# Kernel optimization log

Hardware: AMD Instinct MI355X
Metric: run time of the kernel (lower is better)

## Reference

```python
import jax, jax.numpy as jnp
import numpy as np

N = 4096
DEG = 16.0
KC = 64  # max closed-neighborhood size supported (deg~16 graph => safe)


def setup_inputs() -> dict:
    key = jax.random.key(0)
    ks = jax.random.split(key, 6)
    u = jax.random.uniform(ks[0], (N, N))
    upper = jnp.triu((u < (DEG / N)).astype(jnp.float32), k=1)
    adj = upper + upper.T  # symmetric 0/1, zero diagonal
    d = 64
    return {
        'adj': adj,
        'e_w': jax.random.normal(ks[1], (15, d), dtype=jnp.float32) * 0.25,
        'e_b': jnp.zeros((d,), jnp.float32),
        'w1': jax.random.normal(ks[2], (3, d, d), dtype=jnp.float32) * 0.125,
        'b1': jnp.zeros((3, d), jnp.float32),
        'w2': jax.random.normal(ks[3], (3, d, d), dtype=jnp.float32) * 0.125,
        'b2': jnp.zeros((3, d), jnp.float32),
        'eps': jnp.zeros((3,), jnp.float32),
    }


def cr_feat(adj):
    n = adj.shape[0]
    m = adj + jnp.eye(n, dtype=adj.dtype)  # closed-neighborhood indicator rows [N,N]
    k = m.sum(1)                            # |S_v|
    D = m @ adj                             # D[v,u] = degree of u inside S_v (A symmetric)
    E = 0.5 * jnp.sum(m * D, axis=1)        # edges inside S_v
    W = jnp.sum(m * D * (D - 1.0) * 0.5, axis=1)  # wedges inside S_v
    vals, idx = jax.lax.top_k(m, KC)        # members of S_v (padded)
    valid = (vals > 0.5).astype(adj.dtype)
    sub = adj[idx[:, :, None], idx[:, None, :]]        # [N,KC,KC] induced subgraph
    sub = sub * valid[:, :, None] * valid[:, None, :]
    T = jnp.einsum('vij,vjk,vki->v', sub, sub, sub) / 6.0  # triangles inside S_v
    f3 = T
    f2 = W - 3.0 * T
    f1 = E * (k - 2.0) - 2.0 * f2 - 3.0 * f3
    tot = k * (k - 1.0) * (k - 2.0) / 6.0   # C(k,3) = total triples
    f0 = tot - f1 - f2 - f3
    f = jnp.stack([f0, f1, f2, f3], axis=1)
    f = jnp.where((k >= 3.0)[:, None], f, 0.0)  # original skips |nb|<3
    return f / (jnp.sum(f, axis=1, keepdims=True) + 1e-10)


def ww_feat(adj):
    a2 = adj @ adj
    a4 = a2 @ a2                             # matrix_power(adj, 4)
    vals, _ = jax.lax.top_k(a4, 8)           # per-row sort desc, top 8
    return vals


def degree_feat(adj):
    d = adj.sum(1)
    diag_a2 = jnp.einsum('vu,uv->v', adj, adj)  # diag(A@A)
    return jnp.stack([d, d ** 2, diag_a2], axis=1)


def _forward(adj, e_w, e_b, w1, b1, w2, b2, eps):
    feats = jnp.concatenate([cr_feat(adj), ww_feat(adj), degree_feat(adj)], axis=1)  # [N,15]
    x = feats @ e_w + e_b
    for i in range(3):
        h = (1.0 + eps[i]) * x + adj @ x
        x = jax.nn.relu(h @ w1[i] + b1[i]) @ w2[i] + b2[i]
    return x.sum(0)


def reference(adj, e_w, e_b, w1, b1, w2, b2, eps):
    return _forward(adj, e_w, e_b, w1, b1, w2, b2, eps)
```

## Files before the change

### kernel.cpp

```cpp
#include <hip/hip_runtime.h>
#include <hip/hip_bf16.h>
#include <stdint.h>

#define NN 4096
#define MAXNZ 1536


__global__ __launch_bounds__(256) void scan_k(const float* __restrict__ adj,
                                              int* __restrict__ nbr,
                                              int* __restrict__ deg,
                                              unsigned long long* __restrict__ abits,
                                              float* __restrict__ feats) {
    __shared__ int nlist[4][64];
    int tid = threadIdx.x;
    int wv = tid >> 6, ln = tid & 63;
    int v = blockIdx.x * 4 + wv;
    size_t rb = (size_t)v * NN;
    int total = 0;
    unsigned long long w0 = 0;
    const float4* row4 = (const float4*)(adj + rb);
    for (int base = 0; base < NN; base += 256) {
        float4 f = row4[(base >> 2) + ln];
        int q4 = (base >> 8) << 2;
        #pragma unroll
        for (int j = 0; j < 4; j++) {
            float vj = (j == 0) ? f.x : (j == 1) ? f.y : (j == 2) ? f.z : f.w;
            unsigned long long m = __ballot(vj > 0.5f);
            if (vj > 0.5f) {
                int pos = total + __popcll(m & ((1ull << ln) - 1ull));
                if (pos < 64) nlist[wv][pos] = base + 4 * ln + j;
            }
            if (ln == q4 + j) w0 = m;
            total += __popcll(m);
        }
    }
    abits[(size_t)v * 64 + ln] = w0;
    int degL = min(total, 64);
    if (ln < degL) nbr[v * 64 + ln] = nlist[wv][ln];
    if (ln == 0) {
        deg[v] = total;
        float degf = (float)total;
        feats[v * 16 + 12] = degf;
        feats[v * 16 + 13] = degf * degf;
        feats[v * 16 + 14] = degf;
    }
}

__global__ __launch_bounds__(256) void cra2_k(const unsigned long long* __restrict__ abits,
                                              const int* __restrict__ nbr,
                                              const int* __restrict__ deg,
                                              unsigned int* __restrict__ csr,
                                              int* __restrict__ cnt,
                                              unsigned char* __restrict__ ncb,
                                              float* __restrict__ feats) {
    __shared__ __align__(16) unsigned int smem[NN + 264];
    int tid = threadIdx.x;
    int bid = blockIdx.x;
    int wv = tid >> 6, ln = tid & 63;

    if (bid < NN) {
        unsigned int* acc   = smem;
        int* us             = (int*)(smem + NN);
        int* dus            = (int*)(smem + NN + 64);
        unsigned int* cntS  = smem + NN;
        unsigned int* wsumS = smem + NN + 256;
        int v = bid;
        {
            uint4 z = {0u, 0u, 0u, 0u};
            #pragma unroll
            for (int i = 0; i < 4; i++) ((uint4*)acc)[tid + 256 * i] = z;
        }
        int dv = min(deg[v], 64);
        if (tid < dv) {
            int u = nbr[v * 64 + tid];
            us[tid] = u;
            dus[tid] = min(deg[u], 64);
        }
        __syncthreads();
        for (int p = tid; p < dv * 64; p += 256) {
            int i = p >> 6, wi = p & 63;
            int u = us[i];
            if (wi < dus[i]) atomicAdd(&acc[nbr[u * 64 + wi]], 1u);
        }
        __syncthreads();
        unsigned int local = 0;
        #pragma unroll
        for (int m = 0; m < 16; m++) {
            unsigned int a = acc[tid + 256 * m];
            local += (a + 14u) / 15u;
        }
        int rank = (tid & 31) * 8 + (tid >> 5);
        cntS[rank] = local;
        __syncthreads();
        unsigned int vmy = cntS[tid];
        unsigned int incl = vmy;
        #pragma unroll
        for (int off = 1; off < 64; off <<= 1) {
            unsigned int n = (unsigned int)__shfl_up((int)incl, off, 64);
            if (ln >= off) incl += n;
        }
        if (ln == 63) wsumS[wv] = incl;
        __syncthreads();
        unsigned int wprefix = 0, tot = 0;
        #pragma unroll
        for (int q = 0; q < 4; q++) {
            unsigned int s = wsumS[q];
            if (q < wv) wprefix += s;
            tot += s;
        }
        cntS[tid] = wprefix + (incl - vmy);
        __syncthreads();
        unsigned int pos = cntS[rank];
        unsigned short* dst = (unsigned short*)((char*)csr + (size_t)v * 3072);
        #pragma unroll
        for (int m = 0; m < 16; m++) {
            unsigned int a = acc[tid + 256 * m];
            unsigned int col = (unsigned int)(tid + 256 * m);
            while (a) {
                unsigned int w = a > 15u ? 15u : a;
                if (pos < 1520u) dst[pos] = (unsigned short)((w << 12) | col);
                pos++;
                a -= w;
            }
        }
        unsigned int bs = min(tot, 1520u);
        unsigned int padto = (bs + 7u) & ~7u;
        if (tid < padto - bs) dst[bs + tid] = (unsigned short)(bs + tid);
        if (tid == 0) {
            cnt[v] = (int)bs;
            ncb[v] = (unsigned char)(padto >> 3);
        }
    } else {
        unsigned long long* rows = (unsigned long long*)smem;
        int* mems = (int*)(smem + 1024);
        int v = (bid - NN) * 4 + wv;

        int dv = deg[v];
        int degL = min(dv, 64);
        int c = min(dv + 1, 64);

        int nl = (ln < degL) ? nbr[v * 64 + ln] : 0;
        int isless = (ln < degL && nl < v) ? 1 : 0;
        int pos = isless;
        #pragma unroll
        for (int off = 32; off; off >>= 1) pos += __shfl_xor(pos, off, 64);

        int mem = 0;
        if (ln < c) {
            if (ln < pos)       mem = nl;
            else if (ln == pos) mem = v;
            else                mem = nbr[v * 64 + ln - 1];
        }
        mems[wv * 64 + ln] = mem;
        __syncthreads();

        unsigned long long mask = 0ull;
        {
            const unsigned long long* rowb = abits + (size_t)mem * 64;
            for (int j = 0; j < c; j++) {
                int mj = mems[wv * 64 + j];
                unsigned long long w = rowb[((mj >> 8) << 2) | (mj & 3)];
                mask |= ((w >> ((mj >> 2) & 63)) & 1ull) << j;
            }
        }
        if (ln >= c) mask = 0ull;
        rows[wv * 64 + ln] = mask;
        __syncthreads();

        int tpart = 0;
        float epart = 0.f, wpart = 0.f;
        if (ln < c) {
            unsigned long long mm = mask;
            while (mm) {
                int j = __ffsll(mm) - 1;
                mm &= mm - 1;
                tpart += __popcll(mask & rows[wv * 64 + j]);
            }
            if (ln != pos) {
                int cn = __popcll(rows[wv * 64 + pos] & mask);
                float D2 = (float)cn + 1.0f;
                epart = D2;
                wpart = D2 * (D2 - 1.0f) * 0.5f;
            }
        }
        float es = epart, wsum2 = wpart;
        int ts = tpart;
        #pragma unroll
        for (int off = 32; off; off >>= 1) {
            es += __shfl_xor(es, off, 64);
            wsum2 += __shfl_xor(wsum2, off, 64);
            ts += __shfl_xor(ts, off, 64);
        }

        if (ln == 0) {
            float degf = (float)dv;
            float k = degf + 1.0f;
            float E = 0.5f * (es + degf);
            float W = wsum2 + degf * (degf - 1.0f) * 0.5f;
            float T = (float)ts / 6.0f;
            float f3 = T;
            float f2 = W - 3.0f * T;
            float f1 = E * (k - 2.0f) - 2.0f * f2 - 3.0f * f3;
            float tot2 = k * (k - 1.0f) * (k - 2.0f) / 6.0f;
            float f0 = tot2 - f1 - f2 - f3;
            if (k < 3.0f) { f0 = f1 = f2 = f3 = 0.f; }
            float s = f0 + f1 + f2 + f3 + 1e-10f;
            feats[v * 16 + 0] = f0 / s;
            feats[v * 16 + 1] = f1 / s;
            feats[v * 16 + 2] = f2 / s;
            feats[v * 16 + 3] = f3 / s;
        }
    }
}

__global__ __launch_bounds__(1024) void order_k(const unsigned char* __restrict__ ncb,
                                                int* __restrict__ ord) {
    __shared__ unsigned int bcnt[192];
    __shared__ unsigned int bbase[192];
    int tid = threadIdx.x;
    if (tid < 192) bcnt[tid] = 0u;
    __syncthreads();
    unsigned char myk[4];
    #pragma unroll
    for (int j = 0; j < 4; j++) {
        int v = tid * 4 + j;
        myk[j] = ncb[v];
        atomicAdd(&bcnt[myk[j]], 1u);
    }
    __syncthreads();
    if (tid == 0) {
        unsigned int run = 0;
        for (int b = 191; b >= 0; b--) { bbase[b] = run; run += bcnt[b]; }
    }
    __syncthreads();
    #pragma unroll
    for (int j = 0; j < 4; j++) {
        int v = tid * 4 + j;
        unsigned int p = atomicAdd(&bbase[myk[j]], 1u);
        ord[p] = v;
    }
}

__device__ __forceinline__ void do8(unsigned int* acc, uint4 E, unsigned int W) {
    atomicAdd(&acc[E.x & 0xFFFu],         W * ((E.x >> 12) & 0xFu));
    atomicAdd(&acc[(E.x >> 16) & 0xFFFu], W * (E.x >> 28));
    atomicAdd(&acc[E.y & 0xFFFu],         W * ((E.y >> 12) & 0xFu));
    atomicAdd(&acc[(E.y >> 16) & 0xFFFu], W * (E.y >> 28));
    atomicAdd(&acc[E.z & 0xFFFu],         W * ((E.z >> 12) & 0xFu));
    atomicAdd(&acc[(E.z >> 16) & 0xFFFu], W * (E.z >> 28));
    atomicAdd(&acc[E.w & 0xFFFu],         W * ((E.w >> 12) & 0xFu));
    atomicAdd(&acc[(E.w >> 16) & 0xFFFu], W * (E.w >> 28));
}

__device__ __forceinline__ void do8_1(unsigned int* acc, uint4 E) {
    atomicAdd(&acc[E.x & 0xFFFu],         (E.x >> 12) & 0xFu);
    atomicAdd(&acc[(E.x >> 16) & 0xFFFu], E.x >> 28);
    atomicAdd(&acc[E.y & 0xFFFu],         (E.y >> 12) & 0xFu);
    atomicAdd(&acc[(E.y >> 16) & 0xFFFu], E.y >> 28);
    atomicAdd(&acc[E.z & 0xFFFu],         (E.z >> 12) & 0xFu);
    atomicAdd(&acc[(E.z >> 16) & 0xFFFu], E.z >> 28);
    atomicAdd(&acc[E.w & 0xFFFu],         (E.w >> 12) & 0xFu);
    atomicAdd(&acc[(E.w >> 16) & 0xFFFu], E.w >> 28);
}

__global__ __launch_bounds__(512) void a4row_k(const unsigned int* __restrict__ csr,
                                               const int* __restrict__ cnt,
                                               const unsigned char* __restrict__ ncb,
                                               const int* __restrict__ ord,
                                               const float* __restrict__ feats,
                                               const float* __restrict__ e_w,
                                               const float* __restrict__ e_b,
                                               float* __restrict__ x0) {
    __shared__ unsigned int acc[NN];
    __shared__ __align__(16) unsigned int rowe[MAXNZ];
    __shared__ unsigned int wtops[64];
    int tid = threadIdx.x;
    int wv = tid >> 6, ln = tid & 63;
    int v = ord[blockIdx.x];

    {
        uint4 z = {0u, 0u, 0u, 0u};
        #pragma unroll
        for (int i = 0; i < 2; i++) ((uint4*)acc)[tid + 512 * i] = z;
    }

    int nv = cnt[v];
    int nvp = (nv + 7) & ~7;
    const unsigned short* rowv = (const unsigned short*)((const char*)csr + (size_t)v * 3072);
    for (int i = tid; i < nvp; i += 512) {
        unsigned int e = rowv[i];
        unsigned int u = e & 0xFFFu;
        unsigned int w = e >> 12;
        unsigned int nc = w ? (unsigned int)ncb[u] : 0u;
        rowe[i] = u | (w << 12) | (nc << 16);
    }
    __syncthreads();

    const uint4* csr4 = (const uint4*)csr;
    for (int i0 = wv * 4; i0 < nvp; i0 += 32) {
        uint4 q = *(const uint4*)&rowe[i0];
        int c1 = (int)(q.x >> 16);
        int c2 = c1 + (int)(q.y >> 16);
        int c3 = c2 + (int)(q.z >> 16);
        int tot = c3 + (int)(q.w >> 16);
        unsigned int s0 = ((q.x & 0xFFFu) * 192u)                                 | (((q.x >> 12) & 0xFu) << 21);
        unsigned int s1 = (((q.y & 0xFFFu) * 192u - (unsigned int)c1) & 0x1FFFFFu) | (((q.y >> 12) & 0xFu) << 21);
        unsigned int s2 = (((q.z & 0xFFFu) * 192u - (unsigned int)c2) & 0x1FFFFFu) | (((q.z >> 12) & 0xFu) << 21);
        unsigned int s3 = (((q.w & 0xFFFu) * 192u - (unsigned int)c3) & 0x1FFFFFu) | (((q.w >> 12) & 0xFu) << 21);
        if (((q.x | q.y | q.z | q.w) & 0xF000u) == 0x1000u) {
            for (int g = ln; g < tot; g += 64) {
                unsigned int sel = (g < c1) ? s0 : ((g < c2) ? s1 : ((g < c3) ? s2 : s3));
                unsigned int idx = (sel + (unsigned int)g) & 0x1FFFFFu;
                uint4 E = csr4[idx];
                do8_1(acc, E);
            }
        } else {
            for (int g = ln; g < tot; g += 64) {
                unsigned int sel = (g < c1) ? s0 : ((g < c2) ? s1 : ((g < c3) ? s2 : s3));
                unsigned int idx = (sel + (unsigned int)g) & 0x1FFFFFu;
                uint4 E = csr4[idx];
                do8(acc, E, sel >> 21);
            }
        }
    }
    __syncthreads();

    unsigned int best[8];
    #pragma unroll
    for (int q = 0; q < 8; q++) best[q] = 0u;
    #pragma unroll
    for (int m = 0; m < 8; m++) {
        unsigned int val = acc[tid + 512 * m];
        if (val > best[7]) {
            best[7] = val;
            #pragma unroll
            for (int s = 7; s > 0; s--) {
                if (best[s] > best[s - 1]) {
                    unsigned int t2 = best[s - 1]; best[s - 1] = best[s]; best[s] = t2;
                } else break;
            }
        }
    }

    unsigned int wave_val = 0u;
    #pragma unroll
    for (int r = 0; r < 8; r++) {
        unsigned int m = best[0];
        #pragma unroll
        for (int off = 32; off; off >>= 1)
            m = max(m, (unsigned int)__shfl_xor((int)m, off, 64));
        unsigned long long bb = __ballot(best[0] == m);
        int src = __ffsll(bb) - 1;
        if (ln == src) {
            #pragma unroll
            for (int s = 0; s < 7; s++) best[s] = best[s + 1];
            best[7] = 0u;
        }
        if (ln == r) wave_val = m;
    }
    if (ln < 8) wtops[wv * 8 + ln] = wave_val;
    __syncthreads();

    if (wv == 0) {
        unsigned int cand = wtops[ln];
        unsigned int myv = 0u;
        #pragma unroll
        for (int r = 0; r < 8; r++) {
            unsigned int m = cand;
            #pragma unroll
            for (int off = 32; off; off >>= 1)
                m = max(m, (unsigned int)__shfl_xor((int)m, off, 64));
            unsigned long long bb = __ballot(cand == m);
            int src = __ffsll(bb) - 1;
            if (ln == src) cand = 0u;
            if (ln == r) myv = m;
        }
        int d = ln;
        float s = e_b[d];
        s += feats[v * 16 + 0]  * e_w[0 * 64 + d];
        s += feats[v * 16 + 1]  * e_w[1 * 64 + d];
        s += feats[v * 16 + 2]  * e_w[2 * 64 + d];
        s += feats[v * 16 + 3]  * e_w[3 * 64 + d];
        #pragma unroll
        for (int j = 0; j < 8; j++) {
            float mj = (float)(unsigned int)__shfl((int)myv, j, 64);
            s += mj * e_w[(4 + j) * 64 + d];
        }
        s += feats[v * 16 + 12] * e_w[12 * 64 + d];
        s += feats[v * 16 + 13] * e_w[13 * 64 + d];
        s += feats[v * 16 + 14] * e_w[14 * 64 + d];
        x0[(size_t)v * 64 + d] = s;
    }
}

__global__ __launch_bounds__(256) void layer_k(const float* __restrict__ xin,
                                               float* __restrict__ xout,
                                               const float* __restrict__ w1,
                                               const float* __restrict__ b1,
                                               const float* __restrict__ w2,
                                               const float* __restrict__ b2,
                                               const float* __restrict__ eps,
                                               const int* __restrict__ nbr,
                                               const int* __restrict__ deg,
                                               float* __restrict__ out,
                                               int li) {
    __shared__ float wL[4096];
    __shared__ float h[4][64], t[4][64];
    int tid = threadIdx.x;
    int wv = tid >> 6, d = tid & 63;
    int v = blockIdx.x * 4 + wv;

    {
        const float4* src = (const float4*)(w1 + li * 4096);
        #pragma unroll
        for (int i = 0; i < 4; i++) ((float4*)wL)[tid + 256 * i] = src[tid + 256 * i];
    }

    float xv = xin[(size_t)v * 64 + d];
    int dv = min(deg[v], 64);
    const int* nl = nbr + v * 64;
    float agg = 0.f;
    int j = 0;
    for (; j + 4 <= dv; j += 4) {
        int n0 = nl[j], n1 = nl[j + 1], n2 = nl[j + 2], n3 = nl[j + 3];
        float a0 = xin[(size_t)n0 * 64 + d];
        float a1 = xin[(size_t)n1 * 64 + d];
        float a2v = xin[(size_t)n2 * 64 + d];
        float a3 = xin[(size_t)n3 * 64 + d];
        agg += (a0 + a1) + (a2v + a3);
    }
    for (; j < dv; j++) agg += xin[(size_t)nl[j] * 64 + d];
    float hv = (1.0f + eps[li]) * xv + agg;
    h[wv][d] = hv;
    __syncthreads();

    float s = b1[li * 64 + d];
    #pragma unroll 8
    for (int k = 0; k < 64; k++) s += h[wv][k] * wL[k * 64 + d];
    s = fmaxf(s, 0.f);
    t[wv][d] = s;
    __syncthreads();

    {
        const float4* src = (const float4*)(w2 + li * 4096);
        #pragma unroll
        for (int i = 0; i < 4; i++) ((float4*)wL)[tid + 256 * i] = src[tid + 256 * i];
    }
    __syncthreads();

    float o = b2[li * 64 + d];
    #pragma unroll 8
    for (int k = 0; k < 64; k++) o += t[wv][k] * wL[k * 64 + d];
    if (li == 2) {
        h[wv][d] = o;
        __syncthreads();
        if (wv == 0)
            atomicAdd(&out[d], (h[0][d] + h[1][d]) + (h[2][d] + h[3][d]));
    } else {
        xout[(size_t)v * 64 + d] = o;
    }
}

extern "C" void kernel_launch(void* const* d_in, const int* in_sizes, int n_in,
                              void* d_out, int out_size, void* d_ws, size_t ws_size,
                              hipStream_t stream) {
    const float* adj = (const float*)d_in[0];
    const float* e_w = (const float*)d_in[1];
    const float* e_b = (const float*)d_in[2];
    const float* w1  = (const float*)d_in[3];
    const float* b1  = (const float*)d_in[4];
    const float* w2  = (const float*)d_in[5];
    const float* b2  = (const float*)d_in[6];
    const float* eps = (const float*)d_in[7];
    float* out = (float*)d_out;

    char* ws = (char*)d_ws;
    unsigned int*       csr     = (unsigned int*)(ws);
    int*                nbr     = (int*)(ws + 25165824);
    int*                deg     = (int*)(ws + 26214400);
    int*                cnt     = (int*)(ws + 26230784);
    float*              feats   = (float*)(ws + 26247168);
    float*              x0      = (float*)(ws + 26509312);
    float*              x1      = (float*)(ws + 27557888);
    unsigned long long* abits   = (unsigned long long*)(ws + 28868608);
    unsigned char*      ncb     = (unsigned char*)(ws + 30965760);
    int*                ord     = (int*)(ws + 30969856);

    hipMemsetAsync(out, 0, 64 * sizeof(float), stream);
    scan_k<<<1024, 256, 0, stream>>>(adj, nbr, deg, abits, feats);
    cra2_k<<<5120, 256, 0, stream>>>(abits, nbr, deg, csr, cnt, ncb, feats);
    order_k<<<1, 1024, 0, stream>>>(ncb, ord);
    a4row_k<<<4096, 512, 0, stream>>>(csr, cnt, ncb, ord, feats, e_w, e_b, x0);
    layer_k<<<1024, 256, 0, stream>>>(x0, x1, w1, b1, w2, b2, eps, nbr, deg, out, 0);
    layer_k<<<1024, 256, 0, stream>>>(x1, x0, w1, b1, w2, b2, eps, nbr, deg, out, 1);
    layer_k<<<1024, 256, 0, stream>>>(x0, x1, w1, b1, w2, b2, eps, nbr, deg, out, 2);
}
```

Baseline: 274.4 us.

## Split A² row storage into fixed bucketed region plus overflow for A⁴ gather

The A² CSR row is laid out as 32 fixed-size column buckets of 8 entries (256 uint16), followed by an overflow region and a separate flat list. This lets the A⁴ kernel fetch the fixed 512-byte head of each neighbor row with one uniform uint4 load per half-wave, with no prefix-sum addressing. Only the variable overflow tail goes through the segmented gather, which now processes 8 entries per pass. The work ordering is now based on row count instead of chunk count. The cost is extra padding writes and more complex row building, and the caps of 512 overflow and 768 flat entries could truncate rows on denser graphs.

```diff
diff --git a/kernel.cpp b/kernel.cpp
--- a/kernel.cpp
+++ b/kernel.cpp
@@ -3,7 +3,6 @@
 #include <stdint.h>
 
 #define NN 4096
-#define MAXNZ 1536
 
 
 __global__ __launch_bounds__(256) void scan_k(const float* __restrict__ adj,
@@ -53,17 +52,20 @@
                                               int* __restrict__ cnt,
                                               unsigned char* __restrict__ ncb,
                                               float* __restrict__ feats) {
-    __shared__ __align__(16) unsigned int smem[NN + 264];
+    __shared__ __align__(16) unsigned int smem[NN + 336];
     int tid = threadIdx.x;
     int bid = blockIdx.x;
     int wv = tid >> 6, ln = tid & 63;
 
     if (bid < NN) {
-        unsigned int* acc   = smem;
-        int* us             = (int*)(smem + NN);
-        int* dus            = (int*)(smem + NN + 64);
-        unsigned int* cntS  = smem + NN;
-        unsigned int* wsumS = smem + NN + 256;
+        unsigned int* acc    = smem;
+        int* us              = (int*)(smem + NN);
+        int* dus             = (int*)(smem + NN + 64);
+        unsigned int* cntS   = smem + NN;
+        unsigned int* wsumS  = smem + NN + 256;
+        unsigned int* nS     = smem + NN + 260;
+        unsigned int* oBaseS = smem + NN + 292;
+        unsigned int* ovT    = smem + NN + 324;
         int v = bid;
         {
             uint4 z = {0u, 0u, 0u, 0u};
@@ -110,7 +112,25 @@
         }
         cntS[tid] = wprefix + (incl - vmy);
         __syncthreads();
+        if (tid < 32) {
+            unsigned int base_b = cntS[tid * 8];
+            unsigned int next_b = (tid < 31) ? cntS[tid * 8 + 8] : tot;
+            unsigned int nb = next_b - base_b;
+            nS[tid] = nb;
+            unsigned int ob = nb > 8u ? nb - 8u : 0u;
+            unsigned int inc2 = ob;
+            #pragma unroll
+            for (int off = 1; off < 32; off <<= 1) {
+                unsigned int n2 = (unsigned int)__shfl_up((int)inc2, off, 64);
+                if (ln >= off) inc2 += n2;
+            }
+            oBaseS[tid] = inc2 - ob;
+            if (tid == 31) ovT[0] = inc2;
+        }
+        __syncthreads();
         unsigned int pos = cntS[rank];
+        unsigned int bB  = cntS[(tid & 31) * 8];
+        unsigned int oB  = oBaseS[tid & 31];
         unsigned short* dst = (unsigned short*)((char*)csr + (size_t)v * 3072);
         #pragma unroll
         for (int m = 0; m < 16; m++) {
@@ -118,17 +138,31 @@
             unsigned int col = (unsigned int)(tid + 256 * m);
             while (a) {
                 unsigned int w = a > 15u ? 15u : a;
-                if (pos < 1520u) dst[pos] = (unsigned short)((w << 12) | col);
+                unsigned short ent = (unsigned short)((w << 12) | col);
+                unsigned int j = pos - bB;
+                if (j < 8u) {
+                    dst[(tid & 31) * 8 + j] = ent;
+                } else if (oB + (j - 8u) < 512u) {
+                    dst[256u + oB + (j - 8u)] = ent;
+                }
+                if (pos < 768u) dst[768u + pos] = ent;
                 pos++;
                 a -= w;
             }
         }
-        unsigned int bs = min(tot, 1520u);
+        unsigned int ovTot = min(ovT[0], 512u);
+        unsigned int ovp = (ovTot + 7u) & ~7u;
+        unsigned int bs = min(tot, 768u);
         unsigned int padto = (bs + 7u) & ~7u;
-        if (tid < padto - bs) dst[bs + tid] = (unsigned short)(bs + tid);
+        {
+            unsigned int b2 = (unsigned int)tid >> 3, j2 = (unsigned int)tid & 7u;
+            if (j2 >= nS[b2]) dst[b2 * 8u + j2] = (unsigned short)b2;
+        }
+        if (tid < (int)(ovp - ovTot)) dst[256u + ovTot + tid] = (unsigned short)((ovTot + (unsigned int)tid) & 31u);
+        if (tid < (int)(padto - bs)) dst[768u + bs + tid] = 0;
         if (tid == 0) {
             cnt[v] = (int)bs;
-            ncb[v] = (unsigned char)(padto >> 3);
+            ncb[v] = (unsigned char)(ovp >> 3);
         }
     } else {
         unsigned long long* rows = (unsigned long long*)smem;
@@ -213,7 +247,7 @@
     }
 }
 
-__global__ __launch_bounds__(1024) void order_k(const unsigned char* __restrict__ ncb,
+__global__ __launch_bounds__(1024) void order_k(const int* __restrict__ cnt,
                                                 int* __restrict__ ord) {
     __shared__ unsigned int bcnt[192];
     __shared__ unsigned int bbase[192];
@@ -224,7 +258,7 @@
     #pragma unroll
     for (int j = 0; j < 4; j++) {
         int v = tid * 4 + j;
-        myk[j] = ncb[v];
+        myk[j] = (unsigned char)(min(cnt[v], 767) >> 2);
         atomicAdd(&bcnt[myk[j]], 1u);
     }
     __syncthreads();
@@ -272,7 +306,7 @@
                                                const float* __restrict__ e_b,
                                                float* __restrict__ x0) {
     __shared__ unsigned int acc[NN];
-    __shared__ __align__(16) unsigned int rowe[MAXNZ];
+    __shared__ __align__(16) unsigned int rowe[768];
     __shared__ unsigned int wtops[64];
     int tid = threadIdx.x;
     int wv = tid >> 6, ln = tid & 63;
@@ -286,7 +320,7 @@
 
     int nv = cnt[v];
     int nvp = (nv + 7) & ~7;
-    const unsigned short* rowv = (const unsigned short*)((const char*)csr + (size_t)v * 3072);
+    const unsigned short* rowv = (const unsigned short*)((const char*)csr + (size_t)v * 3072 + 1536);
     for (int i = tid; i < nvp; i += 512) {
         unsigned int e = rowv[i];
         unsigned int u = e & 0xFFFu;
@@ -297,30 +331,44 @@
     __syncthreads();
 
     const uint4* csr4 = (const uint4*)csr;
-    for (int i0 = wv * 4; i0 < nvp; i0 += 32) {
-        uint4 q = *(const uint4*)&rowe[i0];
-        int c1 = (int)(q.x >> 16);
-        int c2 = c1 + (int)(q.y >> 16);
-        int c3 = c2 + (int)(q.z >> 16);
-        int tot = c3 + (int)(q.w >> 16);
-        unsigned int s0 = ((q.x & 0xFFFu) * 192u)                                 | (((q.x >> 12) & 0xFu) << 21);
-        unsigned int s1 = (((q.y & 0xFFFu) * 192u - (unsigned int)c1) & 0x1FFFFFu) | (((q.y >> 12) & 0xFu) << 21);
-        unsigned int s2 = (((q.z & 0xFFFu) * 192u - (unsigned int)c2) & 0x1FFFFFu) | (((q.z >> 12) & 0xFu) << 21);
-        unsigned int s3 = (((q.w & 0xFFFu) * 192u - (unsigned int)c3) & 0x1FFFFFu) | (((q.w >> 12) & 0xFu) << 21);
-        if (((q.x | q.y | q.z | q.w) & 0xF000u) == 0x1000u) {
-            for (int g = ln; g < tot; g += 64) {
-                unsigned int sel = (g < c1) ? s0 : ((g < c2) ? s1 : ((g < c3) ? s2 : s3));
-                unsigned int idx = (sel + (unsigned int)g) & 0x1FFFFFu;
-                uint4 E = csr4[idx];
-                do8_1(acc, E);
-            }
-        } else {
-            for (int g = ln; g < tot; g += 64) {
-                unsigned int sel = (g < c1) ? s0 : ((g < c2) ? s1 : ((g < c3) ? s2 : s3));
-                unsigned int idx = (sel + (unsigned int)g) & 0x1FFFFFu;
-                uint4 E = csr4[idx];
-                do8(acc, E, sel >> 21);
-            }
+
+    int half = ln >> 5, lb = ln & 31;
+    int npair = (nv + 1) >> 1;
+    for (int pi = wv; pi < npair; pi += 8) {
+        int s = 2 * pi + half;
+        unsigned int re = (s < nv) ? rowe[s] : 0u;
+        unsigned int u = re & 0xFFFu;
+        unsigned int W = (re >> 12) & 0xFu;
+        uint4 E = csr4[u * 192u + (unsigned int)lb];
+        if (__ballot(W != 1u) == 0ull) do8_1(acc, E);
+        else                           do8(acc, E, W);
+    }
+
+    for (int i0 = wv * 8; i0 < nvp; i0 += 64) {
+        uint4 qa = *(const uint4*)&rowe[i0];
+        uint4 qb = *(const uint4*)&rowe[i0 + 4];
+        int c1 = (int)(qa.x >> 16);
+        int c2 = c1 + (int)(qa.y >> 16);
+        int c3 = c2 + (int)(qa.z >> 16);
+        int c4 = c3 + (int)(qa.w >> 16);
+        int c5 = c4 + (int)(qb.x >> 16);
+        int c6 = c5 + (int)(qb.y >> 16);
+        int c7 = c6 + (int)(qb.z >> 16);
+        int tot = c7 + (int)(qb.w >> 16);
+        unsigned int s0 = (((qa.x & 0xFFFu) * 192u + 32u)                     & 0x1FFFFFu) | (((qa.x >> 12) & 0xFu) << 21);
+        unsigned int s1 = (((qa.y & 0xFFFu) * 192u + 32u - (unsigned int)c1) & 0x1FFFFFu) | (((qa.y >> 12) & 0xFu) << 21);
+        unsigned int s2 = (((qa.z & 0xFFFu) * 192u + 32u - (unsigned int)c2) & 0x1FFFFFu) | (((qa.z >> 12) & 0xFu) << 21);
+        unsigned int s3 = (((qa.w & 0xFFFu) * 192u + 32u - (unsigned int)c3) & 0x1FFFFFu) | (((qa.w >> 12) & 0xFu) << 21);
+        unsigned int s4 = (((qb.x & 0xFFFu) * 192u + 32u - (unsigned int)c4) & 0x1FFFFFu) | (((qb.x >> 12) & 0xFu) << 21);
+        unsigned int s5 = (((qb.y & 0xFFFu) * 192u + 32u - (unsigned int)c5) & 0x1FFFFFu) | (((qb.y >> 12) & 0xFu) << 21);
+        unsigned int s6 = (((qb.z & 0xFFFu) * 192u + 32u - (unsigned int)c6) & 0x1FFFFFu) | (((qb.z >> 12) & 0xFu) << 21);
+        unsigned int s7 = (((qb.w & 0xFFFu) * 192u + 32u - (unsigned int)c7) & 0x1FFFFFu) | (((qb.w >> 12) & 0xFu) << 21);
+        for (int g = ln; g < tot; g += 64) {
+            unsigned int sel = (g < c1) ? s0 : (g < c2) ? s1 : (g < c3) ? s2 : (g < c4) ? s3
+                             : (g < c5) ? s4 : (g < c6) ? s5 : (g < c7) ? s6 : s7;
+            unsigned int idx = (sel + (unsigned int)g) & 0x1FFFFFu;
+            uint4 E = csr4[idx];
+            do8(acc, E, sel >> 21);
         }
     }
     __syncthreads();
@@ -489,7 +537,7 @@
     hipMemsetAsync(out, 0, 64 * sizeof(float), stream);
     scan_k<<<1024, 256, 0, stream>>>(adj, nbr, deg, abits, feats);
     cra2_k<<<5120, 256, 0, stream>>>(abits, nbr, deg, csr, cnt, ncb, feats);
-    order_k<<<1, 1024, 0, stream>>>(ncb, ord);
+    order_k<<<1, 1024, 0, stream>>>(cnt, ord);
     a4row_k<<<4096, 512, 0, stream>>>(csr, cnt, ncb, ord, feats, e_w, e_b, x0);
     layer_k<<<1024, 256, 0, stream>>>(x0, x1, w1, b1, w2, b2, eps, nbr, deg, out, 0);
     layer_k<<<1024, 256, 0, stream>>>(x1, x0, w1, b1, w2, b2, eps, nbr, deg, out, 1);
```

Result: slower. 281.0 us (+2.4%).
